# Kernel tuning notes

Hardware: AMD Instinct MI355X
Metric: run time of the kernel (lower is better)

## Reference

```python
import jax, jax.numpy as jnp
import numpy as np

D_MODEL = 1024
NUM_HEADS = 16
HEAD_DIM = D_MODEL // NUM_HEADS


def setup_inputs() -> dict:
    key = jax.random.key(0)
    ks = jax.random.split(key, 11)
    B, T, S = 2, 2048, 2048
    s = 1.0 / np.sqrt(D_MODEL)
    return {
        "query": jax.random.normal(ks[0], (B, T, D_MODEL), jnp.float32),
        "key": jax.random.normal(ks[1], (B, S, D_MODEL), jnp.float32),
        "value": jax.random.normal(ks[2], (B, S, D_MODEL), jnp.float32),
        "Wq": jax.random.normal(ks[3], (D_MODEL, D_MODEL), jnp.float32) * s,
        "bq": jnp.zeros((D_MODEL,), jnp.float32),
        "Wk": jax.random.normal(ks[4], (D_MODEL, D_MODEL), jnp.float32) * s,
        "bk": jnp.zeros((D_MODEL,), jnp.float32),
        "Wv": jax.random.normal(ks[5], (D_MODEL, D_MODEL), jnp.float32) * s,
        "bv": jnp.zeros((D_MODEL,), jnp.float32),
        "Wo": jax.random.normal(ks[6], (D_MODEL, D_MODEL), jnp.float32) * s,
        "bo": jnp.zeros((D_MODEL,), jnp.float32),
    }


def reference(query, key, value, Wq, bq, Wk, bk, Wv, bv, Wo, bo):
    B, T, _ = query.shape
    S = key.shape[1]
    # QKV projections (torch Linear: x @ W.T + b)
    q = query @ Wq.T + bq   # [B,T,D]
    k = key @ Wk.T + bk     # [B,S,D]
    v = value @ Wv.T + bv   # [B,S,D]
    # split heads -> [B,H,T,hd]
    q = q.reshape(B, T, NUM_HEADS, HEAD_DIM).transpose(0, 2, 1, 3)
    k = k.reshape(B, S, NUM_HEADS, HEAD_DIM).transpose(0, 2, 1, 3)
    v = v.reshape(B, S, NUM_HEADS, HEAD_DIM).transpose(0, 2, 1, 3)
    # scaled dot-product attention per head (vectorized over all heads)
    scale = 1.0 / jnp.sqrt(jnp.asarray(HEAD_DIM, q.dtype))
    scores = jnp.einsum("bhtd,bhsd->bhts", q, k) * scale  # [B,H,T,S]
    attn = jax.nn.softmax(scores, axis=-1)
    ctx = jnp.einsum("bhts,bhsd->bhtd", attn, v)           # [B,H,T,hd]
    # concat heads -> [B,T,D], then output projection (dropout = identity at eval)
    ctx = ctx.transpose(0, 2, 1, 3).reshape(B, T, D_MODEL)
    return ctx @ Wo.T + bo
```

## Files before the change

kernel.cpp:

```cpp
#include <hip/hip_runtime.h>
#include <hip/hip_bf16.h>
#include <cstdint>
#include <cstddef>

#define D_MODEL 1024
#define NHEADS  16
#define HDIM    64
#define BB      2
#define TT      2048
#define MM      (BB*TT)

typedef __attribute__((ext_vector_type(8)))  short    bf16x8;
typedef __attribute__((ext_vector_type(4)))  float    f32x4;
typedef __attribute__((ext_vector_type(16))) float    f32x16;
typedef __attribute__((ext_vector_type(4)))  unsigned u32x4;
typedef unsigned short u16;

#define QSCALE 0.1803368801111204f


static __device__ __forceinline__ u16 f2bf(float f) {
  unsigned u = __builtin_bit_cast(unsigned, f);
  return (u16)((u + 0x7FFFu + ((u >> 16) & 1u)) >> 16);
}

static __device__ __forceinline__ void async16(const void* g, void* l) {
  __builtin_amdgcn_global_load_lds(
      (__attribute__((address_space(1))) void*)g,
      (__attribute__((address_space(3))) void*)l, 16, 0, 0);
}

static __device__ __forceinline__ unsigned cvtpk(float lo, float hi) {
  __hip_bfloat162 h = __float22bfloat162_rn(float2{lo, hi});
  unsigned r;
  __builtin_memcpy(&r, &h, 4);
  return r;
}


#define NX8 (524288)
#define NW8 (131072)

__global__ __launch_bounds__(256) void cvt_all_kernel(
    const float* __restrict__ q, const float* __restrict__ k,
    const float* __restrict__ v, const float* __restrict__ wq,
    const float* __restrict__ wk, const float* __restrict__ wv,
    const float* __restrict__ wo, u16* __restrict__ dst, int n8) {
  int i = blockIdx.x * 256 + threadIdx.x;
  int stride = gridDim.x * 256;
  for (; i < n8; i += stride) {
    size_t j = (size_t)i;
    const float* s;
    if (j < NX8)            { s = q; }
    else if (j < 2 * NX8)   { s = k;  j -= NX8; }
    else if (j < 3 * NX8)   { s = v;  j -= 2 * (size_t)NX8; }
    else {
      j -= 3 * (size_t)NX8;
      if (j < NW8)          { s = wq; }
      else if (j < 2 * NW8) { s = wk; j -= NW8; }
      else if (j < 3 * NW8) { s = wv; j -= 2 * (size_t)NW8; }
      else                  { s = wo; j -= 3 * (size_t)NW8; }
    }
    float4 a = ((const float4*)s)[2 * j];
    float4 b = ((const float4*)s)[2 * j + 1];
    ushort4 ra, rb;
    ra.x = f2bf(a.x); ra.y = f2bf(a.y); ra.z = f2bf(a.z); ra.w = f2bf(a.w);
    rb.x = f2bf(b.x); rb.y = f2bf(b.y); rb.z = f2bf(b.z); rb.w = f2bf(b.w);
    ((ushort4*)dst)[2 * (size_t)i]     = ra;
    ((ushort4*)dst)[2 * (size_t)i + 1] = rb;
  }
}


static __device__ __forceinline__ void gemm_core_1024(
    const u16* __restrict__ A, const u16* __restrict__ W,
    int m0, int n0, f32x4 acc[4][4], u16* sA, u16* sB) {
  const int tid  = threadIdx.x;
  const int lane = tid & 63;
  const int wave = tid >> 6;
  const int wr = wave >> 1, wc = wave & 1;
  const int l16 = lane & 15, lq = lane >> 4;

  for (int k0 = 0; k0 < D_MODEL; k0 += 64) {
#pragma unroll
    for (int i = 0; i < 4; ++i) {
      int idx = i * 256 + tid;
      int r   = idx >> 3;
      int c8  = (idx & 7) << 3;
      async16(A + (size_t)(m0 + r) * D_MODEL + k0 + c8, sA + idx * 8);
      async16(W + (size_t)(n0 + r) * D_MODEL + k0 + c8, sB + idx * 8);
    }
    __syncthreads();
#pragma unroll
    for (int ks = 0; ks < 2; ++ks) {
      bf16x8 af[4], bfr[4];
#pragma unroll
      for (int mi = 0; mi < 4; ++mi)
        af[mi] = *(const bf16x8*)(sA + (wr*64 + mi*16 + l16)*64 + ks*32 + lq*8);
#pragma unroll
      for (int ni = 0; ni < 4; ++ni)
        bfr[ni] = *(const bf16x8*)(sB + (wc*64 + ni*16 + l16)*64 + ks*32 + lq*8);
#pragma unroll
      for (int mi = 0; mi < 4; ++mi)
#pragma unroll
        for (int ni = 0; ni < 4; ++ni)
          acc[mi][ni] = __builtin_amdgcn_mfma_f32_16x16x32_bf16(
              af[mi], bfr[ni], acc[mi][ni], 0, 0, 0);
    }
    __syncthreads();
  }
}


__global__ __launch_bounds__(256) void qkv_gemm(
    const u16* __restrict__ xq, const u16* __restrict__ xk, const u16* __restrict__ xv,
    const u16* __restrict__ wq, const u16* __restrict__ wk, const u16* __restrict__ wv,
    const float* __restrict__ bq, const float* __restrict__ bk, const float* __restrict__ bv,
    u16* __restrict__ Qo, u16* __restrict__ Ko, u16* __restrict__ Vt) {
  __shared__ __align__(16) u16 sA[128 * 64];
  __shared__ __align__(16) u16 sB[128 * 64];
  const int bid = (blockIdx.x & 7) * 96 + (blockIdx.x >> 3);
  const int mt = bid & 31, ct = bid >> 5;
  const int which = ct >> 3, nt = ct & 7;
  const u16* A = (which == 0) ? xq : (which == 1) ? xk : xv;
  const u16* W = (which == 0) ? wq : (which == 1) ? wk : wv;
  const float* bias = (which == 0) ? bq : (which == 1) ? bk : bv;
  const int m0 = mt * 128, n0 = nt * 128;

  f32x4 acc[4][4];
#pragma unroll
  for (int mi = 0; mi < 4; ++mi)
#pragma unroll
    for (int ni = 0; ni < 4; ++ni)
      acc[mi][ni] = f32x4{0.f, 0.f, 0.f, 0.f};

  gemm_core_1024(A, W, m0, n0, acc, sA, sB);

  const int lane = threadIdx.x & 63, wave = threadIdx.x >> 6;
  const int wr = wave >> 1, wc = wave & 1, l16 = lane & 15, lq = lane >> 4;
  const float qs = (which == 0) ? QSCALE : 1.0f;
#pragma unroll
  for (int mi = 0; mi < 4; ++mi) {
#pragma unroll
    for (int ni = 0; ni < 4; ++ni) {
      int n = n0 + wc*64 + ni*16 + l16;
      float bz = bias[n];
      int mb = m0 + wr*64 + mi*16 + lq*4;
      if (which == 2) {
        int b = mb >> 11, s = mb & 2047;
        ushort4 pk;
        pk.x = f2bf(acc[mi][ni][0] + bz);
        pk.y = f2bf(acc[mi][ni][1] + bz);
        pk.z = f2bf(acc[mi][ni][2] + bz);
        pk.w = f2bf(acc[mi][ni][3] + bz);
        *(ushort4*)(Vt + (size_t)(b * 1024 + n) * 2048 + s) = pk;
      } else {
        u16* O = (which == 0) ? Qo : Ko;
#pragma unroll
        for (int j = 0; j < 4; ++j)
          O[(size_t)(mb + j) * D_MODEL + n] = f2bf((acc[mi][ni][j] + bz) * qs);
      }
    }
  }
}


__global__ __launch_bounds__(256) void attn_kernel(
    const u16* __restrict__ Qb, const u16* __restrict__ Kb,
    const u16* __restrict__ Vt, u16* __restrict__ ctx) {
  __shared__ __align__(16) u16 Kl[2][64][72];
  __shared__ __align__(16) u16 Vl[2][64][72];

  const int bh = blockIdx.x;
  const int b = bh >> 4, h = bh & 15;
  const int qt = blockIdx.y;
  const int tid = threadIdx.x, lane = tid & 63, w = tid >> 6;
  const int l32 = lane & 31, hi = lane >> 5;

  bf16x8 qf[4];
  {
    size_t qrow = (size_t)(b * 2048 + qt * 128 + w * 32 + l32);
#pragma unroll
    for (int t = 0; t < 4; ++t)
      qf[t] = *(const bf16x8*)(Qb + qrow * D_MODEL + h * 64 + t * 16 + hi * 8);
  }

  f32x16 o0 = {0}, o1 = {0};
  float lsumOwn = 0.f;

  const u16* Kg = Kb + (size_t)b * 2048 * D_MODEL + h * 64;
  const u16* Vg = Vt + (size_t)(b * 1024 + h * 64) * 2048;

  const int r0 = tid >> 3,          c0 = (tid & 7) << 3;
  const int r1 = (tid + 256) >> 3,  c1 = c0;

  uint4 kreg0, kreg1, vreg0, vreg1;
  {
    kreg0 = *(const uint4*)(Kg + (size_t)r0 * D_MODEL + c0);
    kreg1 = *(const uint4*)(Kg + (size_t)r1 * D_MODEL + c1);
    vreg0 = *(const uint4*)(Vg + (size_t)r0 * 2048 + c0);
    vreg1 = *(const uint4*)(Vg + (size_t)r1 * 2048 + c1);
  }

  for (int it = 0; it < 32; ++it) {
    const int cur = it & 1;
    *(uint4*)&Kl[cur][r0][c0] = kreg0;
    *(uint4*)&Kl[cur][r1][c1] = kreg1;
    *(uint4*)&Vl[cur][r0][c0] = vreg0;
    *(uint4*)&Vl[cur][r1][c1] = vreg1;

    if (it + 1 < 32) {
      int s0n = (it + 1) * 64;
      kreg0 = *(const uint4*)(Kg + (size_t)(s0n + r0) * D_MODEL + c0);
      kreg1 = *(const uint4*)(Kg + (size_t)(s0n + r1) * D_MODEL + c1);
      vreg0 = *(const uint4*)(Vg + (size_t)r0 * 2048 + s0n + c0);
      vreg1 = *(const uint4*)(Vg + (size_t)r1 * 2048 + s0n + c1);
    }
    __syncthreads();

    f32x16 sa0 = {0}, sa1 = {0};
    __builtin_amdgcn_s_setprio(1);
#pragma unroll
    for (int t = 0; t < 4; ++t) {
      bf16x8 kf0 = *(const bf16x8*)(&Kl[cur][l32][t * 16 + hi * 8]);
      bf16x8 kf1 = *(const bf16x8*)(&Kl[cur][32 + l32][t * 16 + hi * 8]);
      sa0 = __builtin_amdgcn_mfma_f32_32x32x16_bf16(kf0, qf[t], sa0, 0, 0, 0);
      sa1 = __builtin_amdgcn_mfma_f32_32x32x16_bf16(kf1, qf[t], sa1, 0, 0, 0);
    }
    __builtin_amdgcn_s_setprio(0);

    float rs = 0.f;
#pragma unroll
    for (int r = 0; r < 16; ++r) {
      sa0[r] = __builtin_amdgcn_exp2f(sa0[r]);
      sa1[r] = __builtin_amdgcn_exp2f(sa1[r]);
      rs += sa0[r] + sa1[r];
    }
    lsumOwn += rs;

    __builtin_amdgcn_s_setprio(1);
#pragma unroll
    for (int t = 0; t < 4; ++t) {
      const f32x16& sa = (t < 2) ? sa0 : sa1;
      const int rb = 8 * (t & 1);
      u32x4 pw;
      pw[0] = cvtpk(sa[rb + 0], sa[rb + 1]);
      pw[1] = cvtpk(sa[rb + 2], sa[rb + 3]);
      pw[2] = cvtpk(sa[rb + 4], sa[rb + 5]);
      pw[3] = cvtpk(sa[rb + 6], sa[rb + 7]);
      bf16x8 pb = __builtin_bit_cast(bf16x8, pw);

      uint2 a0 = *(const uint2*)(&Vl[cur][l32][t * 16 + hi * 4]);
      uint2 b0 = *(const uint2*)(&Vl[cur][l32][t * 16 + 8 + hi * 4]);
      uint2 a1 = *(const uint2*)(&Vl[cur][32 + l32][t * 16 + hi * 4]);
      uint2 b1 = *(const uint2*)(&Vl[cur][32 + l32][t * 16 + 8 + hi * 4]);
      u32x4 v0; v0[0] = a0.x; v0[1] = a0.y; v0[2] = b0.x; v0[3] = b0.y;
      u32x4 v1; v1[0] = a1.x; v1[1] = a1.y; v1[2] = b1.x; v1[3] = b1.y;
      bf16x8 va0 = __builtin_bit_cast(bf16x8, v0);
      bf16x8 va1 = __builtin_bit_cast(bf16x8, v1);

      o0 = __builtin_amdgcn_mfma_f32_32x32x16_bf16(va0, pb, o0, 0, 0, 0);
      o1 = __builtin_amdgcn_mfma_f32_32x32x16_bf16(va1, pb, o1, 0, 0, 0);
    }
    __builtin_amdgcn_s_setprio(0);
  }

  const float lsum = lsumOwn + __shfl_xor(lsumOwn, 32, 64);
  const float inv = 1.0f / lsum;
  size_t row = (size_t)(b * 2048 + qt * 128 + w * 32 + l32);
  u16* cp = ctx + row * D_MODEL + h * 64;
#pragma unroll
  for (int rq = 0; rq < 4; ++rq) {
    int dbase = 8 * rq + 4 * hi;
    ushort4 pk;
    pk.x = f2bf(o0[4 * rq + 0] * inv);
    pk.y = f2bf(o0[4 * rq + 1] * inv);
    pk.z = f2bf(o0[4 * rq + 2] * inv);
    pk.w = f2bf(o0[4 * rq + 3] * inv);
    *(ushort4*)(cp + dbase) = pk;
    pk.x = f2bf(o1[4 * rq + 0] * inv);
    pk.y = f2bf(o1[4 * rq + 1] * inv);
    pk.z = f2bf(o1[4 * rq + 2] * inv);
    pk.w = f2bf(o1[4 * rq + 3] * inv);
    *(ushort4*)(cp + 32 + dbase) = pk;
  }
}


__global__ __launch_bounds__(256) void out_gemm(
    const u16* __restrict__ ctx, const u16* __restrict__ wo,
    const float* __restrict__ bo, float* __restrict__ out) {
  __shared__ __align__(16) u16 sA[128 * 64];
  __shared__ __align__(16) u16 sB[128 * 64];
  const int bid = (blockIdx.x & 7) * 32 + (blockIdx.x >> 3);
  const int mt = bid & 31, nt = bid >> 5;
  const int m0 = mt * 128, n0 = nt * 128;

  f32x4 acc[4][4];
#pragma unroll
  for (int mi = 0; mi < 4; ++mi)
#pragma unroll
    for (int ni = 0; ni < 4; ++ni)
      acc[mi][ni] = f32x4{0.f, 0.f, 0.f, 0.f};

  gemm_core_1024(ctx, wo, m0, n0, acc, sA, sB);

  const int lane = threadIdx.x & 63, wave = threadIdx.x >> 6;
  const int wr = wave >> 1, wc = wave & 1, l16 = lane & 15, lq = lane >> 4;
#pragma unroll
  for (int mi = 0; mi < 4; ++mi) {
#pragma unroll
    for (int ni = 0; ni < 4; ++ni) {
      int n = n0 + wc*64 + ni*16 + l16;
      float bz = bo[n];
      int mb = m0 + wr*64 + mi*16 + lq*4;
#pragma unroll
      for (int j = 0; j < 4; ++j)
        out[(size_t)(mb + j) * D_MODEL + n] = acc[mi][ni][j] + bz;
    }
  }
}


extern "C" void kernel_launch(void* const* d_in, const int* in_sizes, int n_in,
                              void* d_out, int out_size, void* d_ws, size_t ws_size,
                              hipStream_t stream) {
  const float* query = (const float*)d_in[0];
  const float* key_  = (const float*)d_in[1];
  const float* value = (const float*)d_in[2];
  const float* Wq = (const float*)d_in[3];
  const float* bq = (const float*)d_in[4];
  const float* Wk = (const float*)d_in[5];
  const float* bk = (const float*)d_in[6];
  const float* Wv = (const float*)d_in[7];
  const float* bv = (const float*)d_in[8];
  const float* Wo = (const float*)d_in[9];
  const float* bo = (const float*)d_in[10];
  float* out = (float*)d_out;

  const size_t NX = (size_t)MM * D_MODEL;
  const size_t NW = (size_t)D_MODEL * D_MODEL;

  char* ws = (char*)d_ws;
  u16* xq  = (u16*)ws; ws += NX * 2;
  u16* xk  = (u16*)ws; ws += NX * 2;
  u16* xv  = (u16*)ws; ws += NX * 2;
  u16* wqb = (u16*)ws; ws += NW * 2;
  u16* wkb = (u16*)ws; ws += NW * 2;
  u16* wvb = (u16*)ws; ws += NW * 2;
  u16* wob = (u16*)ws; ws += NW * 2;
  u16* Qb  = (u16*)ws; ws += NX * 2;
  u16* Kb  = (u16*)ws; ws += NX * 2;
  u16* Vtb = (u16*)ws; ws += NX * 2;
  u16* ctx = (u16*)ws; ws += NX * 2;

  const int n8 = 3 * NX8 + 4 * NW8;
  cvt_all_kernel<<<2048, 256, 0, stream>>>(query, key_, value, Wq, Wk, Wv, Wo,
                                           xq, n8);

  qkv_gemm<<<768, 256, 0, stream>>>(xq, xk, xv, wqb, wkb, wvb, bq, bk, bv, Qb, Kb, Vtb);
  attn_kernel<<<dim3(32, 16), 256, 0, stream>>>(Qb, Kb, Vtb, ctx);
  out_gemm<<<256, 256, 0, stream>>>(ctx, wob, bo, out);
}
```

Baseline: 148.3 us.

## Double-buffer LDS tiles in projection GEMMs to overlap loads with MFMA

The shared GEMM core for the QKV and output projections now keeps two LDS buffers per operand. The first K-tile is preloaded before the loop, and each iteration issues async loads for the next tile before running MFMAs on the current one. This is meant to hide global-to-LDS latency behind compute instead of stalling at a barrier before every tile. In exchange, LDS per block doubles from 32KB to 64KB, which may reduce how many blocks fit on each CU, and a dead variable `r` is left in the code.

```diff
diff --git a/kernel.cpp b/kernel.cpp
--- a/kernel.cpp
+++ b/kernel.cpp
@@ -74,32 +74,49 @@
 
 static __device__ __forceinline__ void gemm_core_1024(
     const u16* __restrict__ A, const u16* __restrict__ W,
-    int m0, int n0, f32x4 acc[4][4], u16* sA, u16* sB) {
+    int m0, int n0, f32x4 acc[4][4],
+    u16 (*__restrict__ sA)[128 * 64], u16 (*__restrict__ sB)[128 * 64]) {
   const int tid  = threadIdx.x;
   const int lane = tid & 63;
   const int wave = tid >> 6;
   const int wr = wave >> 1, wc = wave & 1;
   const int l16 = lane & 15, lq = lane >> 4;
 
+  const int r = (tid * 4) >> 3;
+
+#pragma unroll
+  for (int i = 0; i < 4; ++i) {
+    int idx = i * 256 + tid;
+    int rr  = idx >> 3;
+    int c8  = (idx & 7) << 3;
+    async16(A + (size_t)(m0 + rr) * D_MODEL + c8, sA[0] + idx * 8);
+    async16(W + (size_t)(n0 + rr) * D_MODEL + c8, sB[0] + idx * 8);
+  }
+  __syncthreads();
+
+  int cur = 0;
   for (int k0 = 0; k0 < D_MODEL; k0 += 64) {
-#pragma unroll
-    for (int i = 0; i < 4; ++i) {
-      int idx = i * 256 + tid;
-      int r   = idx >> 3;
-      int c8  = (idx & 7) << 3;
-      async16(A + (size_t)(m0 + r) * D_MODEL + k0 + c8, sA + idx * 8);
-      async16(W + (size_t)(n0 + r) * D_MODEL + k0 + c8, sB + idx * 8);
-    }
-    __syncthreads();
+    if (k0 + 64 < D_MODEL) {
+#pragma unroll
+      for (int i = 0; i < 4; ++i) {
+        int idx = i * 256 + tid;
+        int rr  = idx >> 3;
+        int c8  = (idx & 7) << 3;
+        async16(A + (size_t)(m0 + rr) * D_MODEL + k0 + 64 + c8, sA[cur ^ 1] + idx * 8);
+        async16(W + (size_t)(n0 + rr) * D_MODEL + k0 + 64 + c8, sB[cur ^ 1] + idx * 8);
+      }
+    }
+    const u16* a_ = sA[cur];
+    const u16* b_ = sB[cur];
 #pragma unroll
     for (int ks = 0; ks < 2; ++ks) {
       bf16x8 af[4], bfr[4];
 #pragma unroll
       for (int mi = 0; mi < 4; ++mi)
-        af[mi] = *(const bf16x8*)(sA + (wr*64 + mi*16 + l16)*64 + ks*32 + lq*8);
+        af[mi] = *(const bf16x8*)(a_ + (wr*64 + mi*16 + l16)*64 + ks*32 + lq*8);
 #pragma unroll
       for (int ni = 0; ni < 4; ++ni)
-        bfr[ni] = *(const bf16x8*)(sB + (wc*64 + ni*16 + l16)*64 + ks*32 + lq*8);
+        bfr[ni] = *(const bf16x8*)(b_ + (wc*64 + ni*16 + l16)*64 + ks*32 + lq*8);
 #pragma unroll
       for (int mi = 0; mi < 4; ++mi)
 #pragma unroll
@@ -108,7 +125,9 @@
               af[mi], bfr[ni], acc[mi][ni], 0, 0, 0);
     }
     __syncthreads();
-  }
+    cur ^= 1;
+  }
+  (void)r;
 }
 
 
@@ -117,8 +136,8 @@
     const u16* __restrict__ wq, const u16* __restrict__ wk, const u16* __restrict__ wv,
     const float* __restrict__ bq, const float* __restrict__ bk, const float* __restrict__ bv,
     u16* __restrict__ Qo, u16* __restrict__ Ko, u16* __restrict__ Vt) {
-  __shared__ __align__(16) u16 sA[128 * 64];
-  __shared__ __align__(16) u16 sB[128 * 64];
+  __shared__ __align__(16) u16 sA[2][128 * 64];
+  __shared__ __align__(16) u16 sB[2][128 * 64];
   const int bid = (blockIdx.x & 7) * 96 + (blockIdx.x >> 3);
   const int mt = bid & 31, ct = bid >> 5;
   const int which = ct >> 3, nt = ct & 7;
@@ -290,8 +309,8 @@
 __global__ __launch_bounds__(256) void out_gemm(
     const u16* __restrict__ ctx, const u16* __restrict__ wo,
     const float* __restrict__ bo, float* __restrict__ out) {
-  __shared__ __align__(16) u16 sA[128 * 64];
-  __shared__ __align__(16) u16 sB[128 * 64];
+  __shared__ __align__(16) u16 sA[2][128 * 64];
+  __shared__ __align__(16) u16 sB[2][128 * 64];
   const int bid = (blockIdx.x & 7) * 32 + (blockIdx.x >> 3);
   const int mt = bid & 31, nt = bid >> 5;
   const int m0 = mt * 128, n0 = nt * 128;
```

New measurement: 146.8 us. About the same (-1.0%).
